# Performance work log

Measured on AMD Instinct MI355X. Metric: run time of the kernel, lower is better.

Reference implementation:

```python
import jax, jax.numpy as jnp
import numpy as np

N_NODES = 25000
N_EDGES = 400000
D = 128            # input_dim == all gnn_latent_dim entries
N_LAYERS = 3
N_GRAPHS = 512
D_OUT = 10
BN_EPS = 1e-5


def setup_inputs() -> dict:
    key = jax.random.key(0)
    ks = jax.random.split(key, 12)
    s = 1.0 / np.sqrt(D)
    x = jax.random.normal(ks[0], (N_NODES, D), dtype=jnp.float32)
    edge_index = jax.random.randint(ks[1], (2, N_EDGES), 0, N_NODES, dtype=jnp.int64)
    batch = jnp.sort(jax.random.randint(ks[2], (N_NODES,), 0, N_GRAPHS, dtype=jnp.int64))
    W1 = jax.random.normal(ks[3], (N_LAYERS, D, D), dtype=jnp.float32) * s
    b1 = jnp.zeros((N_LAYERS, D), dtype=jnp.float32)
    gamma = jnp.ones((N_LAYERS, D), dtype=jnp.float32)
    beta = jnp.zeros((N_LAYERS, D), dtype=jnp.float32)
    run_mean = jnp.zeros((N_LAYERS, D), dtype=jnp.float32)
    run_var = jnp.ones((N_LAYERS, D), dtype=jnp.float32)
    W2 = jax.random.normal(ks[4], (N_LAYERS, D, D), dtype=jnp.float32) * s
    b2 = jnp.zeros((N_LAYERS, D), dtype=jnp.float32)
    eps = jnp.zeros((N_LAYERS,), dtype=jnp.float32)  # GIN eps, train_eps=True init 0
    Wout = jax.random.normal(ks[5], (D, D_OUT), dtype=jnp.float32) * s
    bout = jnp.zeros((D_OUT,), dtype=jnp.float32)
    return {"x": x, "edge_index": edge_index, "batch": batch,
            "W1": W1, "b1": b1, "gamma": gamma, "beta": beta,
            "run_mean": run_mean, "run_var": run_var,
            "W2": W2, "b2": b2, "eps": eps, "Wout": Wout, "bout": bout}


def reference(x, edge_index, batch, W1, b1, gamma, beta, run_mean, run_var, W2, b2, eps, Wout, bout):
    src, dst = edge_index[0], edge_index[1]
    h = x
    for i in range(N_LAYERS):
        # GIN aggregation: sum_{j in N(i)} h_j + (1 + eps) * h_i  (self loop weight 1+eps)
        agg = jax.ops.segment_sum(h[src], dst, num_segments=N_NODES)
        agg = agg + (1.0 + eps[i]) * h
        # nn: Linear -> BatchNorm1d (eval, running stats) -> ReLU -> Linear
        z = agg @ W1[i] + b1[i]
        z = (z - run_mean[i]) * jax.lax.rsqrt(run_var[i] + BN_EPS) * gamma[i] + beta[i]
        z = jax.nn.relu(z)
        z = z @ W2[i] + b2[i]
        # post-conv activation (dropout p=0 omitted)
        h = jax.nn.relu(z)
    # readout: global mean pool per graph
    ones = jnp.ones((h.shape[0],), dtype=h.dtype)
    counts = jax.ops.segment_sum(ones, batch, num_segments=N_GRAPHS)
    pooled = jax.ops.segment_sum(h, batch, num_segments=N_GRAPHS) / jnp.clip(counts, 1.0)[:, None]
    # single final Linear (fc_latent_dim=[])
    logits = pooled @ Wout + bout
    return logits
```

## Files before the change

### kernel.cpp

```cpp
#include <hip/hip_runtime.h>
#include <hip/hip_bf16.h>

#define NNODES 25000
#define NEDGES 400000
#define DIM 128
#define NGRAPHS 512
#define DOUT 10
#define NPAD 32768

typedef short bf16x8 __attribute__((ext_vector_type(8)));
typedef float f32x4 __attribute__((ext_vector_type(4)));

__device__ inline float bfu_lo(unsigned int u) {
  union { unsigned int i; float f; } v; v.i = u << 16; return v.f;
}
__device__ inline float bfu_hi(unsigned int u) {
  union { unsigned int i; float f; } v; v.i = u & 0xffff0000u; return v.f;
}
__device__ inline unsigned short f2bf(float f) {
  union { float f; unsigned int i; } v; v.f = f;
  unsigned int r = v.i + 0x7fff + ((v.i >> 16) & 1);
  return (unsigned short)(r >> 16);
}


__global__ __launch_bounds__(256) void k_prep(const int* __restrict__ dst,
                                              int* __restrict__ deg,
                                              const float* __restrict__ x,
                                              unsigned short* __restrict__ h0,
                                              const float* __restrict__ W1,
                                              const float* __restrict__ W2,
                                              unsigned short* __restrict__ W1T,
                                              unsigned short* __restrict__ W2T) {
  int b = blockIdx.x;
  if (b < 1563) {
    int i = b * 256 + threadIdx.x;
    if (i < NEDGES) atomicAdd(&deg[dst[i]], 1);
  } else if (b < 3126) {
    int i = (b - 1563) * 256 + threadIdx.x;
    if (i * 8 < NNODES * DIM) {
      const float4* x4 = (const float4*)x;
      float4 a = x4[i * 2], c = x4[i * 2 + 1];
      uint4 p;
      p.x = ((unsigned int)f2bf(a.y) << 16) | f2bf(a.x);
      p.y = ((unsigned int)f2bf(a.w) << 16) | f2bf(a.z);
      p.z = ((unsigned int)f2bf(c.y) << 16) | f2bf(c.x);
      p.w = ((unsigned int)f2bf(c.w) << 16) | f2bf(c.z);
      ((uint4*)h0)[i] = p;
    }
  } else {
    int wb = b - 3126;
    int l = wb >> 1;
    const float* in = ((wb & 1) ? W2 : W1) + (size_t)l * DIM * DIM;
    unsigned short* out = ((wb & 1) ? W2T : W1T) + (size_t)l * DIM * DIM;
    for (int idx = threadIdx.x; idx < DIM * DIM; idx += 256) {
      int c = idx >> 7, k = idx & 127;
      out[idx] = f2bf(in[k * DIM + c]);
    }
  }
}


__global__ __launch_bounds__(1024) void k_scan(const int* __restrict__ deg,
                                               int* __restrict__ offs,
                                               int* __restrict__ cursor) {
  __shared__ int tsum[1024];
  int t = threadIdx.x;
  const int4* d4 = (const int4*)(deg + t * 32);
  int4 v[8];
#pragma unroll
  for (int j = 0; j < 8; ++j) v[j] = d4[j];
  int s = 0;
#pragma unroll
  for (int j = 0; j < 8; ++j) s += v[j].x + v[j].y + v[j].z + v[j].w;
  tsum[t] = s;
  __syncthreads();
  for (int off = 1; off < 1024; off <<= 1) {
    int u = (t >= off) ? tsum[t - off] : 0;
    __syncthreads();
    tsum[t] += u;
    __syncthreads();
  }
  int run = (t == 0) ? 0 : tsum[t - 1];
  int4* o4 = (int4*)(offs + t * 32);
  int4* c4 = (int4*)(cursor + t * 32);
#pragma unroll
  for (int j = 0; j < 8; ++j) {
    int4 w;
    w.x = run; run += v[j].x;
    w.y = run; run += v[j].y;
    w.z = run; run += v[j].z;
    w.w = run; run += v[j].w;
    o4[j] = w; c4[j] = w;
  }
}

__global__ __launch_bounds__(256) void k_scatter(const int* __restrict__ src,
                                                 const int* __restrict__ dst,
                                                 int* __restrict__ cursor,
                                                 int* __restrict__ csr) {
  int i = blockIdx.x * 256 + threadIdx.x;
  if (i < NEDGES) {
    int p = atomicAdd(&cursor[dst[i]], 1);
    csr[p] = src[i];
  }
}


__global__ __launch_bounds__(256) void k_agg(const unsigned short* __restrict__ h,
                                             const int* __restrict__ offs,
                                             const int* __restrict__ csr,
                                             const float* __restrict__ epsp, int layer,
                                             unsigned short* __restrict__ agg) {
  int lane = threadIdx.x & 63;
  int node = blockIdx.x * 4 + (threadIdx.x >> 6);
  const char* hb = (const char*)h;
  unsigned laneB = (unsigned)lane * 4u;
  float eps1 = 1.0f + epsp[layer];
  int s = __builtin_amdgcn_readfirstlane(offs[node]);
  int e = __builtin_amdgcn_readfirstlane(offs[node + 1]);

  unsigned int hv = *(const unsigned int*)(hb + (((unsigned)node << 8) + laneB));
  float a0 = eps1 * bfu_lo(hv), a1 = eps1 * bfu_hi(hv);
  float b0 = 0.f, b1 = 0.f, c0 = 0.f, c1 = 0.f, d0 = 0.f, d1 = 0.f, g0 = 0.f, g1 = 0.f;

  int j = s;
  for (; j + 7 < e; j += 8) {
    unsigned o0 = (unsigned)__builtin_amdgcn_readfirstlane(csr[j + 0]) << 8;
    unsigned o1 = (unsigned)__builtin_amdgcn_readfirstlane(csr[j + 1]) << 8;
    unsigned o2 = (unsigned)__builtin_amdgcn_readfirstlane(csr[j + 2]) << 8;
    unsigned o3 = (unsigned)__builtin_amdgcn_readfirstlane(csr[j + 3]) << 8;
    unsigned o4 = (unsigned)__builtin_amdgcn_readfirstlane(csr[j + 4]) << 8;
    unsigned o5 = (unsigned)__builtin_amdgcn_readfirstlane(csr[j + 5]) << 8;
    unsigned o6 = (unsigned)__builtin_amdgcn_readfirstlane(csr[j + 6]) << 8;
    unsigned o7 = (unsigned)__builtin_amdgcn_readfirstlane(csr[j + 7]) << 8;
    unsigned int v0 = *(const unsigned int*)(hb + (o0 + laneB));
    unsigned int v1 = *(const unsigned int*)(hb + (o1 + laneB));
    unsigned int v2 = *(const unsigned int*)(hb + (o2 + laneB));
    unsigned int v3 = *(const unsigned int*)(hb + (o3 + laneB));
    unsigned int v4 = *(const unsigned int*)(hb + (o4 + laneB));
    unsigned int v5 = *(const unsigned int*)(hb + (o5 + laneB));
    unsigned int v6 = *(const unsigned int*)(hb + (o6 + laneB));
    unsigned int v7 = *(const unsigned int*)(hb + (o7 + laneB));
    a0 += bfu_lo(v0); a1 += bfu_hi(v0);
    b0 += bfu_lo(v1); b1 += bfu_hi(v1);
    c0 += bfu_lo(v2); c1 += bfu_hi(v2);
    d0 += bfu_lo(v3); d1 += bfu_hi(v3);
    g0 += bfu_lo(v4); g1 += bfu_hi(v4);
    a0 += bfu_lo(v5); a1 += bfu_hi(v5);
    b0 += bfu_lo(v6); b1 += bfu_hi(v6);
    c0 += bfu_lo(v7); c1 += bfu_hi(v7);
  }
  for (; j < e; ++j) {
    unsigned o = (unsigned)__builtin_amdgcn_readfirstlane(csr[j]) << 8;
    unsigned int v = *(const unsigned int*)(hb + (o + laneB));
    a0 += bfu_lo(v); a1 += bfu_hi(v);
  }
  a0 += b0 + c0 + d0 + g0;
  a1 += b1 + c1 + d1 + g1;
  ((unsigned int*)agg)[((unsigned)node << 6) + lane] =
      ((unsigned int)f2bf(a1) << 16) | f2bf(a0);
}


#define MROWS 32

__global__ __launch_bounds__(256) void k_mlp(const unsigned short* __restrict__ agg,
                                             const unsigned short* __restrict__ W1T,
                                             const unsigned short* __restrict__ W2T,
                                             const float* __restrict__ b1,
                                             const float* __restrict__ gamma,
                                             const float* __restrict__ beta,
                                             const float* __restrict__ rmean,
                                             const float* __restrict__ rvar,
                                             const float* __restrict__ b2,
                                             unsigned short* __restrict__ hout) {
  __shared__ __align__(16) char smem[MROWS * 256];
  int t = threadIdx.x;
  int lane = t & 63;
  int wv = t >> 6;
  int r0 = blockIdx.x * MROWS;
  int cl = lane & 15;
  int kg = lane >> 4;

  {
    const uint4* ag4 = (const uint4*)(agg + (size_t)r0 * DIM);
#pragma unroll
    for (int it = 0; it < 2; ++it) {
      int u = t + it * 256;
      int row = u >> 4, un = u & 15;
      uint4 v = make_uint4(0u, 0u, 0u, 0u);
      if (r0 + row < NNODES) v = ag4[u];
      *(uint4*)(smem + row * 256 + ((un * 16) ^ ((row & 7) << 4))) = v;
    }
  }

  bf16x8 b1f[2][4], b2f[2][4];
#pragma unroll
  for (int ct = 0; ct < 2; ++ct) {
    int col = wv * 32 + ct * 16 + cl;
    const char* p1 = (const char*)(W1T + (size_t)col * DIM);
    const char* p2 = (const char*)(W2T + (size_t)col * DIM);
#pragma unroll
    for (int kk = 0; kk < 4; ++kk) {
      b1f[ct][kk] = *(const bf16x8*)(p1 + kk * 64 + kg * 16);
      b2f[ct][kk] = *(const bf16x8*)(p2 + kk * 64 + kg * 16);
    }
  }
  float s1c[2], o1c[2], b2c[2];
#pragma unroll
  for (int ct = 0; ct < 2; ++ct) {
    int col = wv * 32 + ct * 16 + cl;
    float sc = gamma[col] * rsqrtf(rvar[col] + 1e-5f);
    s1c[ct] = sc;
    o1c[ct] = (b1[col] - rmean[col]) * sc + beta[col];
    b2c[ct] = b2[col];
  }
  __syncthreads();

  f32x4 zero = {0.f, 0.f, 0.f, 0.f};
  f32x4 acc[2][2] = {{zero, zero}, {zero, zero}};
#pragma unroll
  for (int kk = 0; kk < 4; ++kk) {
#pragma unroll
    for (int rt = 0; rt < 2; ++rt) {
      int row = rt * 16 + cl;
      int un = kk * 4 + kg;
      bf16x8 a = *(const bf16x8*)(smem + row * 256 + ((un * 16) ^ ((row & 7) << 4)));
      acc[rt][0] = __builtin_amdgcn_mfma_f32_16x16x32_bf16(a, b1f[0][kk], acc[rt][0], 0, 0, 0);
      acc[rt][1] = __builtin_amdgcn_mfma_f32_16x16x32_bf16(a, b1f[1][kk], acc[rt][1], 0, 0, 0);
    }
  }
  __syncthreads();

#pragma unroll
  for (int rt = 0; rt < 2; ++rt)
#pragma unroll
    for (int ct = 0; ct < 2; ++ct) {
      int col = wv * 32 + ct * 16 + cl;
#pragma unroll
      for (int j = 0; j < 4; ++j) {
        int row = rt * 16 + kg * 4 + j;
        float z = fmaxf(acc[rt][ct][j] * s1c[ct] + o1c[ct], 0.f);
        *(unsigned short*)(smem + row * 256 + ((col * 2) ^ ((row & 7) << 4))) = f2bf(z);
      }
    }
  __syncthreads();

  f32x4 acc2[2][2] = {{zero, zero}, {zero, zero}};
#pragma unroll
  for (int kk = 0; kk < 4; ++kk) {
#pragma unroll
    for (int rt = 0; rt < 2; ++rt) {
      int row = rt * 16 + cl;
      int un = kk * 4 + kg;
      bf16x8 a = *(const bf16x8*)(smem + row * 256 + ((un * 16) ^ ((row & 7) << 4)));
      acc2[rt][0] = __builtin_amdgcn_mfma_f32_16x16x32_bf16(a, b2f[0][kk], acc2[rt][0], 0, 0, 0);
      acc2[rt][1] = __builtin_amdgcn_mfma_f32_16x16x32_bf16(a, b2f[1][kk], acc2[rt][1], 0, 0, 0);
    }
  }
  __syncthreads();

#pragma unroll
  for (int rt = 0; rt < 2; ++rt)
#pragma unroll
    for (int ct = 0; ct < 2; ++ct) {
      int col = wv * 32 + ct * 16 + cl;
#pragma unroll
      for (int j = 0; j < 4; ++j) {
        int row = rt * 16 + kg * 4 + j;
        float hv = fmaxf(acc2[rt][ct][j] + b2c[ct], 0.f);
        *(unsigned short*)(smem + row * 256 + ((col * 2) ^ ((row & 7) << 4))) = f2bf(hv);
      }
    }
  __syncthreads();

  {
    uint4* ho4 = (uint4*)(hout + (size_t)r0 * DIM);
#pragma unroll
    for (int it = 0; it < 2; ++it) {
      int u = t + it * 256;
      int row = u >> 4, un = u & 15;
      if (r0 + row < NNODES) {
        uint4 v = *(const uint4*)(smem + row * 256 + ((un * 16) ^ ((row & 7) << 4)));
        ho4[u] = v;
      }
    }
  }
}


__device__ inline int lower_bound_i(const int* a, int n, int key) {
  int lo = 0, hi = n;
  while (lo < hi) {
    int m = (lo + hi) >> 1;
    if (a[m] < key) lo = m + 1; else hi = m;
  }
  return lo;
}

__global__ __launch_bounds__(256) void k_pool(const unsigned short* __restrict__ h,
                                              const int* __restrict__ batch,
                                              const float* __restrict__ Wout,
                                              const float* __restrict__ bout,
                                              float* __restrict__ out) {
  int g = blockIdx.x;
  int t = threadIdx.x;
  int cg = t & 31;
  int st = t >> 5;
  int lo = lower_bound_i(batch, NNODES, g);
  int hi = lower_bound_i(batch, NNODES, g + 1);
  const uint2* h2 = (const uint2*)h;
  float a0 = 0.f, a1 = 0.f, a2 = 0.f, a3 = 0.f;
  for (int i = lo + st; i < hi; i += 8) {
    uint2 v = h2[(size_t)i * 32 + cg];
    a0 += bfu_lo(v.x); a1 += bfu_hi(v.x); a2 += bfu_lo(v.y); a3 += bfu_hi(v.y);
  }
  __shared__ float red[8][DIM];
  __shared__ float pooled[DIM];
  red[st][cg * 4 + 0] = a0; red[st][cg * 4 + 1] = a1;
  red[st][cg * 4 + 2] = a2; red[st][cg * 4 + 3] = a3;
  __syncthreads();
  if (t < DIM) {
    float s = 0.f;
#pragma unroll
    for (int k = 0; k < 8; ++k) s += red[k][t];
    float cnt = (hi > lo) ? (float)(hi - lo) : 1.0f;
    pooled[t] = s / cnt;
  }
  __syncthreads();
  if (t < DOUT) {
    float acc = bout[t];
#pragma unroll 8
    for (int k = 0; k < DIM; ++k) acc = fmaf(pooled[k], Wout[k * DOUT + t], acc);
    out[g * DOUT + t] = acc;
  }
}


extern "C" void kernel_launch(void* const* d_in, const int* in_sizes, int n_in,
                              void* d_out, int out_size, void* d_ws, size_t ws_size,
                              hipStream_t stream) {
  const float* x     = (const float*)d_in[0];
  const int*   ei    = (const int*)d_in[1];
  const int*   batch = (const int*)d_in[2];
  const float* W1    = (const float*)d_in[3];
  const float* b1    = (const float*)d_in[4];
  const float* gamma = (const float*)d_in[5];
  const float* beta  = (const float*)d_in[6];
  const float* rmean = (const float*)d_in[7];
  const float* rvar  = (const float*)d_in[8];
  const float* W2    = (const float*)d_in[9];
  const float* b2    = (const float*)d_in[10];
  const float* eps   = (const float*)d_in[11];
  const float* Wout  = (const float*)d_in[12];
  const float* bout  = (const float*)d_in[13];
  float* out = (float*)d_out;

  const int* src = ei;
  const int* dst = ei + NEDGES;

  char* ws = (char*)d_ws;
  size_t o = 0;
  auto alloc = [&](size_t bytes) -> void* {
    o = (o + 255) & ~(size_t)255;
    void* p = ws + o;
    o += bytes;
    return p;
  };
  int* deg    = (int*)alloc(NPAD * sizeof(int));
  int* offs   = (int*)alloc((NPAD + 8) * sizeof(int));
  int* cursor = (int*)alloc(NPAD * sizeof(int));
  int* csr    = (int*)alloc(NEDGES * sizeof(int));
  unsigned short* h0  = (unsigned short*)alloc((size_t)NNODES * DIM * 2);
  unsigned short* agg = (unsigned short*)alloc((size_t)NNODES * DIM * 2);
  unsigned short* hA  = (unsigned short*)alloc((size_t)NNODES * DIM * 2);
  unsigned short* hB  = (unsigned short*)alloc((size_t)NNODES * DIM * 2);
  unsigned short* W1T = (unsigned short*)alloc(3 * DIM * DIM * 2);
  unsigned short* W2T = (unsigned short*)alloc(3 * DIM * DIM * 2);

  hipMemsetAsync(deg, 0, NPAD * sizeof(int), stream);
  k_prep<<<3132, 256, 0, stream>>>(dst, deg, x, h0, W1, W2, W1T, W2T);
  k_scan<<<1, 1024, 0, stream>>>(deg, offs, cursor);
  k_scatter<<<(NEDGES + 255) / 256, 256, 0, stream>>>(src, dst, cursor, csr);

  const unsigned short* hin = h0;
  unsigned short* houts[3] = {hA, hB, hA};
  for (int l = 0; l < 3; ++l) {
    k_agg<<<NNODES / 4, 256, 0, stream>>>(hin, offs, csr, eps, l, agg);
    k_mlp<<<(NNODES + MROWS - 1) / MROWS, 256, 0, stream>>>(
        agg, W1T + (size_t)l * DIM * DIM, W2T + (size_t)l * DIM * DIM,
        b1 + l * DIM, gamma + l * DIM, beta + l * DIM, rmean + l * DIM,
        rvar + l * DIM, b2 + l * DIM, houts[l]);
    hin = houts[l];
  }
  k_pool<<<NGRAPHS, 256, 0, stream>>>(hin, batch, Wout, bout, out);
}
```

Before: 247.5 us.

## Fuse all stages into one persistent cooperative kernel with grid syncs

Replaces the sequence of separate launches (memset, prep, scan, scatter, per-layer agg/mlp, pool) with one cooperative persistent kernel that separates phases with grid-wide syncs. Degree counting and cursor atomics are spread across 8 replicated histogram copies to reduce atomic contention, and the single-block scan becomes a two-level multi-block scan. The goal is to remove launch gaps and tail effects. In exchange it adds grid.sync costs, grid-stride loops with limited resident blocks, and register pressure from launch_bounds(256,4).

```diff
diff --git a/kernel.cpp b/kernel.cpp
--- a/kernel.cpp
+++ b/kernel.cpp
@@ -1,5 +1,8 @@
 #include <hip/hip_runtime.h>
 #include <hip/hip_bf16.h>
+#include <hip/hip_cooperative_groups.h>
+
+namespace cg = cooperative_groups;
 
 #define NNODES 25000
 #define NEDGES 400000
@@ -7,6 +10,8 @@
 #define NGRAPHS 512
 #define DOUT 10
 #define NPAD 32768
+#define NCOPY 8
+#define MTILES ((NNODES + 31) / 32)
 
 typedef short bf16x8 __attribute__((ext_vector_type(8)));
 typedef float f32x4 __attribute__((ext_vector_type(4)));
@@ -23,23 +28,45 @@
   return (unsigned short)(r >> 16);
 }
 
-
-__global__ __launch_bounds__(256) void k_prep(const int* __restrict__ dst,
-                                              int* __restrict__ deg,
-                                              const float* __restrict__ x,
-                                              unsigned short* __restrict__ h0,
-                                              const float* __restrict__ W1,
-                                              const float* __restrict__ W2,
-                                              unsigned short* __restrict__ W1T,
-                                              unsigned short* __restrict__ W2T) {
-  int b = blockIdx.x;
-  if (b < 1563) {
-    int i = b * 256 + threadIdx.x;
-    if (i < NEDGES) atomicAdd(&deg[dst[i]], 1);
-  } else if (b < 3126) {
-    int i = (b - 1563) * 256 + threadIdx.x;
-    if (i * 8 < NNODES * DIM) {
-      const float4* x4 = (const float4*)x;
+__device__ inline int lower_bound_i(const int* a, int n, int key) {
+  int lo = 0, hi = n;
+  while (lo < hi) {
+    int m = (lo + hi) >> 1;
+    if (a[m] < key) lo = m + 1; else hi = m;
+  }
+  return lo;
+}
+
+__global__ __launch_bounds__(256, 4) void k_mega(
+    const int* __restrict__ src, const int* __restrict__ dst,
+    const float* __restrict__ x, const int* __restrict__ batch,
+    const float* __restrict__ W1, const float* __restrict__ b1,
+    const float* __restrict__ gamma, const float* __restrict__ beta,
+    const float* __restrict__ rmean, const float* __restrict__ rvar,
+    const float* __restrict__ W2, const float* __restrict__ b2,
+    const float* __restrict__ epsv, const float* __restrict__ Wout,
+    const float* __restrict__ bout, float* __restrict__ out,
+    int* __restrict__ deg8, int* __restrict__ cursor8, int* __restrict__ offs,
+    int* __restrict__ csr, int* __restrict__ blocksum,
+    unsigned short* __restrict__ h0, unsigned short* __restrict__ aggbuf,
+    unsigned short* __restrict__ hA, unsigned short* __restrict__ hB,
+    unsigned short* __restrict__ W1T, unsigned short* __restrict__ W2T) {
+  cg::grid_group grid = cg::this_grid();
+  __shared__ __align__(16) char smem[8192];
+  const int t = threadIdx.x;
+  const int blk = blockIdx.x;
+  const int nb = gridDim.x;
+  const int gtid = blk * 256 + t;
+  const int stride = nb * 256;
+
+  for (int i = gtid; i < NCOPY * NPAD; i += stride) deg8[i] = 0;
+  grid.sync();
+
+  {
+    int* dp = deg8 + (size_t)(blk & (NCOPY - 1)) * NPAD;
+    for (int i = gtid; i < NEDGES; i += stride) atomicAdd(&dp[dst[i]], 1);
+    const float4* x4 = (const float4*)x;
+    for (int i = gtid; i < NNODES * DIM / 8; i += stride) {
       float4 a = x4[i * 2], c = x4[i * 2 + 1];
       uint4 p;
       p.x = ((unsigned int)f2bf(a.y) << 16) | f2bf(a.x);
@@ -48,292 +75,285 @@
       p.w = ((unsigned int)f2bf(c.w) << 16) | f2bf(c.z);
       ((uint4*)h0)[i] = p;
     }
-  } else {
-    int wb = b - 3126;
-    int l = wb >> 1;
-    const float* in = ((wb & 1) ? W2 : W1) + (size_t)l * DIM * DIM;
-    unsigned short* out = ((wb & 1) ? W2T : W1T) + (size_t)l * DIM * DIM;
-    for (int idx = threadIdx.x; idx < DIM * DIM; idx += 256) {
-      int c = idx >> 7, k = idx & 127;
-      out[idx] = f2bf(in[k * DIM + c]);
-    }
-  }
-}
-
-
-__global__ __launch_bounds__(1024) void k_scan(const int* __restrict__ deg,
-                                               int* __restrict__ offs,
-                                               int* __restrict__ cursor) {
-  __shared__ int tsum[1024];
-  int t = threadIdx.x;
-  const int4* d4 = (const int4*)(deg + t * 32);
-  int4 v[8];
-#pragma unroll
-  for (int j = 0; j < 8; ++j) v[j] = d4[j];
-  int s = 0;
-#pragma unroll
-  for (int j = 0; j < 8; ++j) s += v[j].x + v[j].y + v[j].z + v[j].w;
-  tsum[t] = s;
-  __syncthreads();
-  for (int off = 1; off < 1024; off <<= 1) {
-    int u = (t >= off) ? tsum[t - off] : 0;
+    for (int i = gtid; i < 6 * DIM * DIM; i += stride) {
+      int m = i >> 14, idx = i & 16383;
+      int l = m >> 1;
+      const float* win = ((m & 1) ? W2 : W1) + (size_t)l * DIM * DIM;
+      unsigned short* wout = ((m & 1) ? W2T : W1T) + (size_t)l * DIM * DIM;
+      int cc = idx >> 7, kk = idx & 127;
+      wout[idx] = f2bf(win[kk * DIM + cc]);
+    }
+  }
+  grid.sync();
+
+  int* ismem = (int*)smem;
+  if (blk < 32) {
+    int n0 = blk * 1024 + t * 4;
+    int4 tot = make_int4(0, 0, 0, 0);
+#pragma unroll
+    for (int c = 0; c < NCOPY; ++c) {
+      int4 v = *(const int4*)(deg8 + (size_t)c * NPAD + n0);
+      tot.x += v.x; tot.y += v.y; tot.z += v.z; tot.w += v.w;
+    }
+    int ts = tot.x + tot.y + tot.z + tot.w;
+    ismem[t] = ts;
     __syncthreads();
-    tsum[t] += u;
-    __syncthreads();
-  }
-  int run = (t == 0) ? 0 : tsum[t - 1];
-  int4* o4 = (int4*)(offs + t * 32);
-  int4* c4 = (int4*)(cursor + t * 32);
-#pragma unroll
-  for (int j = 0; j < 8; ++j) {
-    int4 w;
-    w.x = run; run += v[j].x;
-    w.y = run; run += v[j].y;
-    w.z = run; run += v[j].z;
-    w.w = run; run += v[j].w;
-    o4[j] = w; c4[j] = w;
-  }
-}
-
-__global__ __launch_bounds__(256) void k_scatter(const int* __restrict__ src,
-                                                 const int* __restrict__ dst,
-                                                 int* __restrict__ cursor,
-                                                 int* __restrict__ csr) {
-  int i = blockIdx.x * 256 + threadIdx.x;
-  if (i < NEDGES) {
-    int p = atomicAdd(&cursor[dst[i]], 1);
-    csr[p] = src[i];
-  }
-}
-
-
-__global__ __launch_bounds__(256) void k_agg(const unsigned short* __restrict__ h,
-                                             const int* __restrict__ offs,
-                                             const int* __restrict__ csr,
-                                             const float* __restrict__ epsp, int layer,
-                                             unsigned short* __restrict__ agg) {
-  int lane = threadIdx.x & 63;
-  int node = blockIdx.x * 4 + (threadIdx.x >> 6);
-  const char* hb = (const char*)h;
-  unsigned laneB = (unsigned)lane * 4u;
-  float eps1 = 1.0f + epsp[layer];
-  int s = __builtin_amdgcn_readfirstlane(offs[node]);
-  int e = __builtin_amdgcn_readfirstlane(offs[node + 1]);
-
-  unsigned int hv = *(const unsigned int*)(hb + (((unsigned)node << 8) + laneB));
-  float a0 = eps1 * bfu_lo(hv), a1 = eps1 * bfu_hi(hv);
-  float b0 = 0.f, b1 = 0.f, c0 = 0.f, c1 = 0.f, d0 = 0.f, d1 = 0.f, g0 = 0.f, g1 = 0.f;
-
-  int j = s;
-  for (; j + 7 < e; j += 8) {
-    unsigned o0 = (unsigned)__builtin_amdgcn_readfirstlane(csr[j + 0]) << 8;
-    unsigned o1 = (unsigned)__builtin_amdgcn_readfirstlane(csr[j + 1]) << 8;
-    unsigned o2 = (unsigned)__builtin_amdgcn_readfirstlane(csr[j + 2]) << 8;
-    unsigned o3 = (unsigned)__builtin_amdgcn_readfirstlane(csr[j + 3]) << 8;
-    unsigned o4 = (unsigned)__builtin_amdgcn_readfirstlane(csr[j + 4]) << 8;
-    unsigned o5 = (unsigned)__builtin_amdgcn_readfirstlane(csr[j + 5]) << 8;
-    unsigned o6 = (unsigned)__builtin_amdgcn_readfirstlane(csr[j + 6]) << 8;
-    unsigned o7 = (unsigned)__builtin_amdgcn_readfirstlane(csr[j + 7]) << 8;
-    unsigned int v0 = *(const unsigned int*)(hb + (o0 + laneB));
-    unsigned int v1 = *(const unsigned int*)(hb + (o1 + laneB));
-    unsigned int v2 = *(const unsigned int*)(hb + (o2 + laneB));
-    unsigned int v3 = *(const unsigned int*)(hb + (o3 + laneB));
-    unsigned int v4 = *(const unsigned int*)(hb + (o4 + laneB));
-    unsigned int v5 = *(const unsigned int*)(hb + (o5 + laneB));
-    unsigned int v6 = *(const unsigned int*)(hb + (o6 + laneB));
-    unsigned int v7 = *(const unsigned int*)(hb + (o7 + laneB));
-    a0 += bfu_lo(v0); a1 += bfu_hi(v0);
-    b0 += bfu_lo(v1); b1 += bfu_hi(v1);
-    c0 += bfu_lo(v2); c1 += bfu_hi(v2);
-    d0 += bfu_lo(v3); d1 += bfu_hi(v3);
-    g0 += bfu_lo(v4); g1 += bfu_hi(v4);
-    a0 += bfu_lo(v5); a1 += bfu_hi(v5);
-    b0 += bfu_lo(v6); b1 += bfu_hi(v6);
-    c0 += bfu_lo(v7); c1 += bfu_hi(v7);
-  }
-  for (; j < e; ++j) {
-    unsigned o = (unsigned)__builtin_amdgcn_readfirstlane(csr[j]) << 8;
-    unsigned int v = *(const unsigned int*)(hb + (o + laneB));
-    a0 += bfu_lo(v); a1 += bfu_hi(v);
-  }
-  a0 += b0 + c0 + d0 + g0;
-  a1 += b1 + c1 + d1 + g1;
-  ((unsigned int*)agg)[((unsigned)node << 6) + lane] =
-      ((unsigned int)f2bf(a1) << 16) | f2bf(a0);
-}
-
-
-#define MROWS 32
-
-__global__ __launch_bounds__(256) void k_mlp(const unsigned short* __restrict__ agg,
-                                             const unsigned short* __restrict__ W1T,
-                                             const unsigned short* __restrict__ W2T,
-                                             const float* __restrict__ b1,
-                                             const float* __restrict__ gamma,
-                                             const float* __restrict__ beta,
-                                             const float* __restrict__ rmean,
-                                             const float* __restrict__ rvar,
-                                             const float* __restrict__ b2,
-                                             unsigned short* __restrict__ hout) {
-  __shared__ __align__(16) char smem[MROWS * 256];
-  int t = threadIdx.x;
-  int lane = t & 63;
-  int wv = t >> 6;
-  int r0 = blockIdx.x * MROWS;
-  int cl = lane & 15;
-  int kg = lane >> 4;
+    for (int off = 1; off < 256; off <<= 1) {
+      int u = (t >= off) ? ismem[t - off] : 0;
+      __syncthreads();
+      ismem[t] += u;
+      __syncthreads();
+    }
+    int excl = ismem[t] - ts;
+    int4 o;
+    o.x = excl; o.y = o.x + tot.x; o.z = o.y + tot.y; o.w = o.z + tot.z;
+    *(int4*)(offs + n0) = o;
+    if (t == 255) blocksum[blk] = ismem[255];
+  }
+  grid.sync();
+
+  if (blk < 32) {
+    int bb = 0;
+    for (int b2i = 0; b2i < blk; ++b2i) bb += blocksum[b2i];
+    int n0 = blk * 1024 + t * 4;
+    int4 lo4 = *(const int4*)(offs + n0);
+    lo4.x += bb; lo4.y += bb; lo4.z += bb; lo4.w += bb;
+    *(int4*)(offs + n0) = lo4;
+    int c0 = lo4.x, c1 = lo4.y, c2 = lo4.z, c3 = lo4.w;
+#pragma unroll
+    for (int c = 0; c < NCOPY; ++c) {
+      int4 v = *(const int4*)(deg8 + (size_t)c * NPAD + n0);
+      int* cur = cursor8 + (size_t)c * NPAD + n0;
+      cur[0] = c0; c0 += v.x;
+      cur[1] = c1; c1 += v.y;
+      cur[2] = c2; c2 += v.z;
+      cur[3] = c3; c3 += v.w;
+    }
+  }
+  grid.sync();
 
   {
-    const uint4* ag4 = (const uint4*)(agg + (size_t)r0 * DIM);
-#pragma unroll
-    for (int it = 0; it < 2; ++it) {
-      int u = t + it * 256;
-      int row = u >> 4, un = u & 15;
-      uint4 v = make_uint4(0u, 0u, 0u, 0u);
-      if (r0 + row < NNODES) v = ag4[u];
-      *(uint4*)(smem + row * 256 + ((un * 16) ^ ((row & 7) << 4))) = v;
-    }
-  }
-
-  bf16x8 b1f[2][4], b2f[2][4];
-#pragma unroll
-  for (int ct = 0; ct < 2; ++ct) {
-    int col = wv * 32 + ct * 16 + cl;
-    const char* p1 = (const char*)(W1T + (size_t)col * DIM);
-    const char* p2 = (const char*)(W2T + (size_t)col * DIM);
-#pragma unroll
-    for (int kk = 0; kk < 4; ++kk) {
-      b1f[ct][kk] = *(const bf16x8*)(p1 + kk * 64 + kg * 16);
-      b2f[ct][kk] = *(const bf16x8*)(p2 + kk * 64 + kg * 16);
-    }
-  }
-  float s1c[2], o1c[2], b2c[2];
-#pragma unroll
-  for (int ct = 0; ct < 2; ++ct) {
-    int col = wv * 32 + ct * 16 + cl;
-    float sc = gamma[col] * rsqrtf(rvar[col] + 1e-5f);
-    s1c[ct] = sc;
-    o1c[ct] = (b1[col] - rmean[col]) * sc + beta[col];
-    b2c[ct] = b2[col];
-  }
-  __syncthreads();
-
-  f32x4 zero = {0.f, 0.f, 0.f, 0.f};
-  f32x4 acc[2][2] = {{zero, zero}, {zero, zero}};
-#pragma unroll
-  for (int kk = 0; kk < 4; ++kk) {
-#pragma unroll
-    for (int rt = 0; rt < 2; ++rt) {
-      int row = rt * 16 + cl;
-      int un = kk * 4 + kg;
-      bf16x8 a = *(const bf16x8*)(smem + row * 256 + ((un * 16) ^ ((row & 7) << 4)));
-      acc[rt][0] = __builtin_amdgcn_mfma_f32_16x16x32_bf16(a, b1f[0][kk], acc[rt][0], 0, 0, 0);
-      acc[rt][1] = __builtin_amdgcn_mfma_f32_16x16x32_bf16(a, b1f[1][kk], acc[rt][1], 0, 0, 0);
-    }
-  }
-  __syncthreads();
-
-#pragma unroll
-  for (int rt = 0; rt < 2; ++rt)
-#pragma unroll
-    for (int ct = 0; ct < 2; ++ct) {
-      int col = wv * 32 + ct * 16 + cl;
-#pragma unroll
-      for (int j = 0; j < 4; ++j) {
-        int row = rt * 16 + kg * 4 + j;
-        float z = fmaxf(acc[rt][ct][j] * s1c[ct] + o1c[ct], 0.f);
-        *(unsigned short*)(smem + row * 256 + ((col * 2) ^ ((row & 7) << 4))) = f2bf(z);
-      }
-    }
-  __syncthreads();
-
-  f32x4 acc2[2][2] = {{zero, zero}, {zero, zero}};
-#pragma unroll
-  for (int kk = 0; kk < 4; ++kk) {
-#pragma unroll
-    for (int rt = 0; rt < 2; ++rt) {
-      int row = rt * 16 + cl;
-      int un = kk * 4 + kg;
-      bf16x8 a = *(const bf16x8*)(smem + row * 256 + ((un * 16) ^ ((row & 7) << 4)));
-      acc2[rt][0] = __builtin_amdgcn_mfma_f32_16x16x32_bf16(a, b2f[0][kk], acc2[rt][0], 0, 0, 0);
-      acc2[rt][1] = __builtin_amdgcn_mfma_f32_16x16x32_bf16(a, b2f[1][kk], acc2[rt][1], 0, 0, 0);
-    }
-  }
-  __syncthreads();
-
-#pragma unroll
-  for (int rt = 0; rt < 2; ++rt)
-#pragma unroll
-    for (int ct = 0; ct < 2; ++ct) {
-      int col = wv * 32 + ct * 16 + cl;
-#pragma unroll
-      for (int j = 0; j < 4; ++j) {
-        int row = rt * 16 + kg * 4 + j;
-        float hv = fmaxf(acc2[rt][ct][j] + b2c[ct], 0.f);
-        *(unsigned short*)(smem + row * 256 + ((col * 2) ^ ((row & 7) << 4))) = f2bf(hv);
-      }
-    }
-  __syncthreads();
+    int* cur = cursor8 + (size_t)(blk & (NCOPY - 1)) * NPAD;
+    for (int i = gtid; i < NEDGES; i += stride) {
+      int p = atomicAdd(&cur[dst[i]], 1);
+      csr[p] = src[i];
+    }
+  }
+  grid.sync();
+
+  const int lane = t & 63;
+  const int wv = t >> 6;
+  const int cl = lane & 15;
+  const int kg = lane >> 4;
+  const unsigned laneB = (unsigned)lane * 4u;
+  const unsigned short* hin = h0;
+
+  for (int l = 0; l < 3; ++l) {
+    {
+      const char* hb = (const char*)hin;
+      float eps1 = 1.0f + epsv[l];
+      for (int node = blk * 4 + wv; node < NNODES; node += nb * 4) {
+        int s = __builtin_amdgcn_readfirstlane(offs[node]);
+        int e = __builtin_amdgcn_readfirstlane(offs[node + 1]);
+        unsigned int hv = *(const unsigned int*)(hb + (((unsigned)node << 8) + laneB));
+        float a0 = eps1 * bfu_lo(hv), a1 = eps1 * bfu_hi(hv);
+        float p0 = 0.f, p1 = 0.f, q0 = 0.f, q1 = 0.f;
+        float r0f = 0.f, r1f = 0.f, u0 = 0.f, u1 = 0.f;
+        int j = s;
+        for (; j + 7 < e; j += 8) {
+          unsigned o0 = (unsigned)__builtin_amdgcn_readfirstlane(csr[j + 0]) << 8;
+          unsigned o1 = (unsigned)__builtin_amdgcn_readfirstlane(csr[j + 1]) << 8;
+          unsigned o2 = (unsigned)__builtin_amdgcn_readfirstlane(csr[j + 2]) << 8;
+          unsigned o3 = (unsigned)__builtin_amdgcn_readfirstlane(csr[j + 3]) << 8;
+          unsigned o4 = (unsigned)__builtin_amdgcn_readfirstlane(csr[j + 4]) << 8;
+          unsigned o5 = (unsigned)__builtin_amdgcn_readfirstlane(csr[j + 5]) << 8;
+          unsigned o6 = (unsigned)__builtin_amdgcn_readfirstlane(csr[j + 6]) << 8;
+          unsigned o7 = (unsigned)__builtin_amdgcn_readfirstlane(csr[j + 7]) << 8;
+          unsigned int v0 = *(const unsigned int*)(hb + (o0 + laneB));
+          unsigned int v1 = *(const unsigned int*)(hb + (o1 + laneB));
+          unsigned int v2 = *(const unsigned int*)(hb + (o2 + laneB));
+          unsigned int v3 = *(const unsigned int*)(hb + (o3 + laneB));
+          unsigned int v4 = *(const unsigned int*)(hb + (o4 + laneB));
+          unsigned int v5 = *(const unsigned int*)(hb + (o5 + laneB));
+          unsigned int v6 = *(const unsigned int*)(hb + (o6 + laneB));
+          unsigned int v7 = *(const unsigned int*)(hb + (o7 + laneB));
+          a0 += bfu_lo(v0); a1 += bfu_hi(v0);
+          p0 += bfu_lo(v1); p1 += bfu_hi(v1);
+          q0 += bfu_lo(v2); q1 += bfu_hi(v2);
+          r0f += bfu_lo(v3); r1f += bfu_hi(v3);
+          u0 += bfu_lo(v4); u1 += bfu_hi(v4);
+          a0 += bfu_lo(v5); a1 += bfu_hi(v5);
+          p0 += bfu_lo(v6); p1 += bfu_hi(v6);
+          q0 += bfu_lo(v7); q1 += bfu_hi(v7);
+        }
+        for (; j < e; ++j) {
+          unsigned o = (unsigned)__builtin_amdgcn_readfirstlane(csr[j]) << 8;
+          unsigned int v = *(const unsigned int*)(hb + (o + laneB));
+          a0 += bfu_lo(v); a1 += bfu_hi(v);
+        }
+        a0 += p0 + q0 + r0f + u0;
+        a1 += p1 + q1 + r1f + u1;
+        ((unsigned int*)aggbuf)[((unsigned)node << 6) + lane] =
+            ((unsigned int)f2bf(a1) << 16) | f2bf(a0);
+      }
+    }
+    grid.sync();
+
+    {
+      const unsigned short* lW1T = W1T + (size_t)l * DIM * DIM;
+      const unsigned short* lW2T = W2T + (size_t)l * DIM * DIM;
+      const float* lb1 = b1 + l * DIM;
+      const float* lg = gamma + l * DIM;
+      const float* lbe = beta + l * DIM;
+      const float* lrm = rmean + l * DIM;
+      const float* lrv = rvar + l * DIM;
+      const float* lb2 = b2 + l * DIM;
+      unsigned short* hout = (l == 1) ? hB : hA;
+
+      bf16x8 b1f[2][4], b2f[2][4];
+      float s1c[2], o1c[2], b2c[2];
+#pragma unroll
+      for (int ct = 0; ct < 2; ++ct) {
+        int col = wv * 32 + ct * 16 + cl;
+        const char* p1 = (const char*)(lW1T + (size_t)col * DIM);
+        const char* p2 = (const char*)(lW2T + (size_t)col * DIM);
+#pragma unroll
+        for (int kk = 0; kk < 4; ++kk) {
+          b1f[ct][kk] = *(const bf16x8*)(p1 + kk * 64 + kg * 16);
+          b2f[ct][kk] = *(const bf16x8*)(p2 + kk * 64 + kg * 16);
+        }
+        float sc = lg[col] * rsqrtf(lrv[col] + 1e-5f);
+        s1c[ct] = sc;
+        o1c[ct] = (lb1[col] - lrm[col]) * sc + lbe[col];
+        b2c[ct] = lb2[col];
+      }
+
+      for (int tile = blk; tile < MTILES; tile += nb) {
+        int r0 = tile * 32;
+        {
+          const uint4* ag4 = (const uint4*)(aggbuf + (size_t)r0 * DIM);
+#pragma unroll
+          for (int it = 0; it < 2; ++it) {
+            int u = t + it * 256;
+            int row = u >> 4, un = u & 15;
+            uint4 v = make_uint4(0u, 0u, 0u, 0u);
+            if (r0 + row < NNODES) v = ag4[u];
+            *(uint4*)(smem + row * 256 + ((un * 16) ^ ((row & 7) << 4))) = v;
+          }
+        }
+        __syncthreads();
+
+        f32x4 zero = {0.f, 0.f, 0.f, 0.f};
+        f32x4 acc[2][2] = {{zero, zero}, {zero, zero}};
+#pragma unroll
+        for (int kk = 0; kk < 4; ++kk) {
+#pragma unroll
+          for (int rt = 0; rt < 2; ++rt) {
+            int row = rt * 16 + cl;
+            int un = kk * 4 + kg;
+            bf16x8 a = *(const bf16x8*)(smem + row * 256 + ((un * 16) ^ ((row & 7) << 4)));
+            acc[rt][0] = __builtin_amdgcn_mfma_f32_16x16x32_bf16(a, b1f[0][kk], acc[rt][0], 0, 0, 0);
+            acc[rt][1] = __builtin_amdgcn_mfma_f32_16x16x32_bf16(a, b1f[1][kk], acc[rt][1], 0, 0, 0);
+          }
+        }
+        __syncthreads();
+
+#pragma unroll
+        for (int rt = 0; rt < 2; ++rt)
+#pragma unroll
+          for (int ct = 0; ct < 2; ++ct) {
+            int col = wv * 32 + ct * 16 + cl;
+#pragma unroll
+            for (int j = 0; j < 4; ++j) {
+              int row = rt * 16 + kg * 4 + j;
+              float z = fmaxf(acc[rt][ct][j] * s1c[ct] + o1c[ct], 0.f);
+              *(unsigned short*)(smem + row * 256 + ((col * 2) ^ ((row & 7) << 4))) = f2bf(z);
+            }
+          }
+        __syncthreads();
+
+        f32x4 acc2[2][2] = {{zero, zero}, {zero, zero}};
+#pragma unroll
+        for (int kk = 0; kk < 4; ++kk) {
+#pragma unroll
+          for (int rt = 0; rt < 2; ++rt) {
+            int row = rt * 16 + cl;
+            int un = kk * 4 + kg;
+            bf16x8 a = *(const bf16x8*)(smem + row * 256 + ((un * 16) ^ ((row & 7) << 4)));
+            acc2[rt][0] = __builtin_amdgcn_mfma_f32_16x16x32_bf16(a, b2f[0][kk], acc2[rt][0], 0, 0, 0);
+            acc2[rt][1] = __builtin_amdgcn_mfma_f32_16x16x32_bf16(a, b2f[1][kk], acc2[rt][1], 0, 0, 0);
+          }
+        }
+        __syncthreads();
+
+#pragma unroll
+        for (int rt = 0; rt < 2; ++rt)
+#pragma unroll
+          for (int ct = 0; ct < 2; ++ct) {
+            int col = wv * 32 + ct * 16 + cl;
+#pragma unroll
+            for (int j = 0; j < 4; ++j) {
+              int row = rt * 16 + kg * 4 + j;
+              float hv = fmaxf(acc2[rt][ct][j] + b2c[ct], 0.f);
+              *(unsigned short*)(smem + row * 256 + ((col * 2) ^ ((row & 7) << 4))) = f2bf(hv);
+            }
+          }
+        __syncthreads();
+
+        {
+          uint4* ho4 = (uint4*)(hout + (size_t)r0 * DIM);
+#pragma unroll
+          for (int it = 0; it < 2; ++it) {
+            int u = t + it * 256;
+            int row = u >> 4, un = u & 15;
+            if (r0 + row < NNODES) {
+              uint4 v = *(const uint4*)(smem + row * 256 + ((un * 16) ^ ((row & 7) << 4)));
+              ho4[u] = v;
+            }
+          }
+        }
+        __syncthreads();
+      }
+    }
+    grid.sync();
+    hin = (l == 1) ? hB : hA;
+  }
 
   {
-    uint4* ho4 = (uint4*)(hout + (size_t)r0 * DIM);
-#pragma unroll
-    for (int it = 0; it < 2; ++it) {
-      int u = t + it * 256;
-      int row = u >> 4, un = u & 15;
-      if (r0 + row < NNODES) {
-        uint4 v = *(const uint4*)(smem + row * 256 + ((un * 16) ^ ((row & 7) << 4)));
-        ho4[u] = v;
-      }
-    }
-  }
-}
-
-
-__device__ inline int lower_bound_i(const int* a, int n, int key) {
-  int lo = 0, hi = n;
-  while (lo < hi) {
-    int m = (lo + hi) >> 1;
-    if (a[m] < key) lo = m + 1; else hi = m;
-  }
-  return lo;
-}
-
-__global__ __launch_bounds__(256) void k_pool(const unsigned short* __restrict__ h,
-                                              const int* __restrict__ batch,
-                                              const float* __restrict__ Wout,
-                                              const float* __restrict__ bout,
-                                              float* __restrict__ out) {
-  int g = blockIdx.x;
-  int t = threadIdx.x;
-  int cg = t & 31;
-  int st = t >> 5;
-  int lo = lower_bound_i(batch, NNODES, g);
-  int hi = lower_bound_i(batch, NNODES, g + 1);
-  const uint2* h2 = (const uint2*)h;
-  float a0 = 0.f, a1 = 0.f, a2 = 0.f, a3 = 0.f;
-  for (int i = lo + st; i < hi; i += 8) {
-    uint2 v = h2[(size_t)i * 32 + cg];
-    a0 += bfu_lo(v.x); a1 += bfu_hi(v.x); a2 += bfu_lo(v.y); a3 += bfu_hi(v.y);
-  }
-  __shared__ float red[8][DIM];
-  __shared__ float pooled[DIM];
-  red[st][cg * 4 + 0] = a0; red[st][cg * 4 + 1] = a1;
-  red[st][cg * 4 + 2] = a2; red[st][cg * 4 + 3] = a3;
-  __syncthreads();
-  if (t < DIM) {
-    float s = 0.f;
-#pragma unroll
-    for (int k = 0; k < 8; ++k) s += red[k][t];
-    float cnt = (hi > lo) ? (float)(hi - lo) : 1.0f;
-    pooled[t] = s / cnt;
-  }
-  __syncthreads();
-  if (t < DOUT) {
-    float acc = bout[t];
+    float* red = (float*)smem;
+    float* pooled = (float*)(smem + 4096);
+    const uint2* h2 = (const uint2*)hin;
+    int cg2 = t & 31;
+    int st = t >> 5;
+    for (int g = blk; g < NGRAPHS; g += nb) {
+      int lo = lower_bound_i(batch, NNODES, g);
+      int hi = lower_bound_i(batch, NNODES, g + 1);
+      float a0 = 0.f, a1 = 0.f, a2 = 0.f, a3 = 0.f;
+      for (int i = lo + st; i < hi; i += 8) {
+        uint2 v = h2[(size_t)i * 32 + cg2];
+        a0 += bfu_lo(v.x); a1 += bfu_hi(v.x); a2 += bfu_lo(v.y); a3 += bfu_hi(v.y);
+      }
+      red[st * DIM + cg2 * 4 + 0] = a0;
+      red[st * DIM + cg2 * 4 + 1] = a1;
+      red[st * DIM + cg2 * 4 + 2] = a2;
+      red[st * DIM + cg2 * 4 + 3] = a3;
+      __syncthreads();
+      if (t < DIM) {
+        float s = 0.f;
+#pragma unroll
+        for (int k = 0; k < 8; ++k) s += red[k * DIM + t];
+        float cnt = (hi > lo) ? (float)(hi - lo) : 1.0f;
+        pooled[t] = s / cnt;
+      }
+      __syncthreads();
+      if (t < DOUT) {
+        float acc = bout[t];
 #pragma unroll 8
-    for (int k = 0; k < DIM; ++k) acc = fmaf(pooled[k], Wout[k * DOUT + t], acc);
-    out[g * DOUT + t] = acc;
+        for (int k = 0; k < DIM; ++k) acc = fmaf(pooled[k], Wout[k * DOUT + t], acc);
+        out[g * DOUT + t] = acc;
+      }
+      __syncthreads();
+    }
   }
 }
 
@@ -341,9 +361,10 @@
 extern "C" void kernel_launch(void* const* d_in, const int* in_sizes, int n_in,
                               void* d_out, int out_size, void* d_ws, size_t ws_size,
                               hipStream_t stream) {
+  const int* src     = (const int*)d_in[1];
+  const int* dst     = ((const int*)d_in[1]) + NEDGES;
   const float* x     = (const float*)d_in[0];
-  const int*   ei    = (const int*)d_in[1];
-  const int*   batch = (const int*)d_in[2];
+  const int* batch   = (const int*)d_in[2];
   const float* W1    = (const float*)d_in[3];
   const float* b1    = (const float*)d_in[4];
   const float* gamma = (const float*)d_in[5];
@@ -352,13 +373,10 @@
   const float* rvar  = (const float*)d_in[8];
   const float* W2    = (const float*)d_in[9];
   const float* b2    = (const float*)d_in[10];
-  const float* eps   = (const float*)d_in[11];
+  const float* epsv  = (const float*)d_in[11];
   const float* Wout  = (const float*)d_in[12];
   const float* bout  = (const float*)d_in[13];
   float* out = (float*)d_out;
-
-  const int* src = ei;
-  const int* dst = ei + NEDGES;
 
   char* ws = (char*)d_ws;
   size_t o = 0;
@@ -368,31 +386,35 @@
     o += bytes;
     return p;
   };
-  int* deg    = (int*)alloc(NPAD * sizeof(int));
-  int* offs   = (int*)alloc((NPAD + 8) * sizeof(int));
-  int* cursor = (int*)alloc(NPAD * sizeof(int));
-  int* csr    = (int*)alloc(NEDGES * sizeof(int));
-  unsigned short* h0  = (unsigned short*)alloc((size_t)NNODES * DIM * 2);
-  unsigned short* agg = (unsigned short*)alloc((size_t)NNODES * DIM * 2);
-  unsigned short* hA  = (unsigned short*)alloc((size_t)NNODES * DIM * 2);
-  unsigned short* hB  = (unsigned short*)alloc((size_t)NNODES * DIM * 2);
-  unsigned short* W1T = (unsigned short*)alloc(3 * DIM * DIM * 2);
-  unsigned short* W2T = (unsigned short*)alloc(3 * DIM * DIM * 2);
-
-  hipMemsetAsync(deg, 0, NPAD * sizeof(int), stream);
-  k_prep<<<3132, 256, 0, stream>>>(dst, deg, x, h0, W1, W2, W1T, W2T);
-  k_scan<<<1, 1024, 0, stream>>>(deg, offs, cursor);
-  k_scatter<<<(NEDGES + 255) / 256, 256, 0, stream>>>(src, dst, cursor, csr);
-
-  const unsigned short* hin = h0;
-  unsigned short* houts[3] = {hA, hB, hA};
-  for (int l = 0; l < 3; ++l) {
-    k_agg<<<NNODES / 4, 256, 0, stream>>>(hin, offs, csr, eps, l, agg);
-    k_mlp<<<(NNODES + MROWS - 1) / MROWS, 256, 0, stream>>>(
-        agg, W1T + (size_t)l * DIM * DIM, W2T + (size_t)l * DIM * DIM,
-        b1 + l * DIM, gamma + l * DIM, beta + l * DIM, rmean + l * DIM,
-        rvar + l * DIM, b2 + l * DIM, houts[l]);
-    hin = houts[l];
-  }
-  k_pool<<<NGRAPHS, 256, 0, stream>>>(hin, batch, Wout, bout, out);
-}
+  int* deg8     = (int*)alloc((size_t)NCOPY * NPAD * sizeof(int));
+  int* cursor8  = (int*)alloc((size_t)NCOPY * NPAD * sizeof(int));
+  int* offs     = (int*)alloc((NPAD + 8) * sizeof(int));
+  int* csr      = (int*)alloc(NEDGES * sizeof(int));
+  int* blocksum = (int*)alloc(64 * sizeof(int));
+  unsigned short* h0     = (unsigned short*)alloc((size_t)NNODES * DIM * 2);
+  unsigned short* aggbuf = (unsigned short*)alloc((size_t)NNODES * DIM * 2);
+  unsigned short* hA     = (unsigned short*)alloc((size_t)NNODES * DIM * 2);
+  unsigned short* hB     = (unsigned short*)alloc((size_t)NNODES * DIM * 2);
+  unsigned short* W1T    = (unsigned short*)alloc(3 * DIM * DIM * 2);
+  unsigned short* W2T    = (unsigned short*)alloc(3 * DIM * DIM * 2);
+
+  int maxb = 0;
+  hipError_t qerr =
+      hipOccupancyMaxActiveBlocksPerMultiprocessor(&maxb, (const void*)k_mega, 256, 0);
+  if (qerr != hipSuccess || maxb < 1) maxb = 4;
+  long long nblk_ll = (long long)maxb * 256;
+  int nblk = (nblk_ll > 2048) ? 2048 : (int)nblk_ll;
+  if (nblk < 32) nblk = 32;
+
+  void* args[] = {
+      (void*)&src, (void*)&dst, (void*)&x, (void*)&batch,
+      (void*)&W1, (void*)&b1, (void*)&gamma, (void*)&beta,
+      (void*)&rmean, (void*)&rvar, (void*)&W2, (void*)&b2,
+      (void*)&epsv, (void*)&Wout, (void*)&bout, (void*)&out,
+      (void*)&deg8, (void*)&cursor8, (void*)&offs, (void*)&csr, (void*)&blocksum,
+      (void*)&h0, (void*)&aggbuf, (void*)&hA, (void*)&hB,
+      (void*)&W1T, (void*)&W2T};
+
+  hipLaunchCooperativeKernel((const void*)k_mega, dim3(nblk), dim3(256), args, 0,
+                             stream);
+}
```

Result: slower. 921.2 us (+272.2%).
